# Optimization experiments

Hardware: AMD Instinct MI355X
Metric: run time of the kernel (lower is better)

## Reference

```python
import jax, jax.numpy as jnp
import numpy as np

H_SPLITS = [2, 3, 3]          # crpe_window {3:2, 5:3, 7:3}
K_SIZES = [3, 5, 7]
NUM_HEADS = 8
EPS = 1e-6


def dwconv(x, w, b, k):
    # x: (B,C,H,W), w: (C,1,k,k) depthwise, 'same' padding
    y = jax.lax.conv_general_dilated(
        x, w, (1, 1), [(k // 2, k // 2)] * 2,
        feature_group_count=x.shape[1],
        dimension_numbers=('NCHW', 'OIHW', 'NCHW'))
    return y + b[None, :, None, None]


def layernorm(x, g, b):
    m = jnp.mean(x, -1, keepdims=True)
    v = jnp.var(x, -1, keepdims=True)
    return (x - m) * jax.lax.rsqrt(v + EPS) * g + b


def conv_rel_pos_enc(q, v, ws, bs, H, W):
    # ConvRelPosEnc (MPViT style, no cls token): q * depthwise_conv(v)
    B, h, N, Ch = q.shape
    v_img = v.transpose(0, 1, 3, 2).reshape(B, h * Ch, H, W)  # B (h Ch) H W
    splits = np.cumsum([hs * Ch for hs in H_SPLITS])[:-1]
    parts = jnp.split(v_img, splits, axis=1)
    conv_v = jnp.concatenate(
        [dwconv(p, w, b, k) for p, w, b, k in zip(parts, ws, bs, K_SIZES)], axis=1)
    conv_v = conv_v.reshape(B, h, Ch, N).transpose(0, 1, 3, 2)
    return q * conv_v


def setup_inputs() -> dict:
    key = jax.random.key(0)
    B, H, W, C, nd, r, mr = 8, 64, 64, 320, 4, 2, 4
    h = NUM_HEADS
    N = H * W
    Ch = C // h
    hid = C // r
    ks = jax.random.split(key, 16)
    s = 0.02
    return {
        'x': jax.random.normal(ks[0], (B, N, C), jnp.float32),
        'domain_label': jax.nn.one_hot(jax.random.randint(ks[1], (B,), 0, nd), nd, dtype=jnp.float32),
        'cpe_w': jax.random.normal(ks[2], (C, 1, 3, 3), jnp.float32) * s,
        'cpe_b': jnp.zeros((C,), jnp.float32),
        'ln1_g': jnp.ones((C,), jnp.float32), 'ln1_b': jnp.zeros((C,), jnp.float32),
        'qkv_w': jax.random.normal(ks[3], (3 * C, C), jnp.float32) * s,
        'qkv_b': jnp.zeros((3 * C,), jnp.float32),
        'crpe_w3': jax.random.normal(ks[4], (2 * Ch, 1, 3, 3), jnp.float32) * s,
        'crpe_b3': jnp.zeros((2 * Ch,), jnp.float32),
        'crpe_w5': jax.random.normal(ks[5], (3 * Ch, 1, 5, 5), jnp.float32) * s,
        'crpe_b5': jnp.zeros((3 * Ch,), jnp.float32),
        'crpe_w7': jax.random.normal(ks[6], (3 * Ch, 1, 7, 7), jnp.float32) * s,
        'crpe_b7': jnp.zeros((3 * Ch,), jnp.float32),
        'dom_w1': jax.random.normal(ks[7], (hid, nd), jnp.float32) * s,
        'dom_b1': jnp.zeros((hid,), jnp.float32),
        'dom_w2': jax.random.normal(ks[8], (C, hid), jnp.float32) * s,
        'dom_b2': jnp.zeros((C,), jnp.float32),
        'proj_w': jax.random.normal(ks[9], (C, C), jnp.float32) * s,
        'proj_b': jnp.zeros((C,), jnp.float32),
        'ln2_g': jnp.ones((C,), jnp.float32), 'ln2_b': jnp.zeros((C,), jnp.float32),
        'mlp_w1': jax.random.normal(ks[10], (mr * C, C), jnp.float32) * s,
        'mlp_b1': jnp.zeros((mr * C,), jnp.float32),
        'mlp_w2': jax.random.normal(ks[11], (C, mr * C), jnp.float32) * s,
        'mlp_b2': jnp.zeros((C,), jnp.float32),
        'H': H, 'W': W,
    }


def reference(x, domain_label, cpe_w, cpe_b, ln1_g, ln1_b, qkv_w, qkv_b,
              crpe_w3, crpe_b3, crpe_w5, crpe_b5, crpe_w7, crpe_b7,
              dom_w1, dom_b1, dom_w2, dom_b2, proj_w, proj_b,
              ln2_g, ln2_b, mlp_w1, mlp_b1, mlp_w2, mlp_b2, H, W):
    B, N, C = x.shape
    h = NUM_HEADS
    Ch = C // h
    scale = Ch ** -0.5
    # ConvPosEnc: depthwise 3x3 conv + residual
    img = x.transpose(0, 2, 1).reshape(B, C, H, W)
    x = (dwconv(img, cpe_w, cpe_b, 3) + img).reshape(B, C, N).transpose(0, 2, 1)
    # FactorAtt_ConvRelPosEnc_Sup
    cur = layernorm(x, ln1_g, ln1_b)
    qkv = (cur @ qkv_w.T + qkv_b).reshape(B, N, 3, h, Ch).transpose(2, 0, 3, 1, 4)
    q, k, v = qkv[0], qkv[1], qkv[2]          # (B,h,N,Ch) each
    k_sm = jax.nn.softmax(k, axis=2)          # softmax over tokens
    kv = jnp.einsum('bhnk,bhnv->bhkv', k_sm, v)   # (B,h,Ch,Ch)
    fa = jnp.einsum('bhnk,bhkv->bhnv', q, kv)
    fa = scale * fa + conv_rel_pos_enc(
        q, v, (crpe_w3, crpe_w5, crpe_w7), (crpe_b3, crpe_b5, crpe_b7), H, W)
    # domain gate: MLP(one_hot) -> softmax over heads, broadcast over tokens
    d = jax.nn.relu(domain_label @ dom_w1.T + dom_b1) @ dom_w2.T + dom_b2  # (B,C)
    d = jax.nn.softmax(d.reshape(B, h, 1, Ch), axis=1)
    att = (d * fa).transpose(0, 2, 1, 3).reshape(B, N, C)
    x = x + (att @ proj_w.T + proj_b)
    # MLP (GELU, ratio 4)
    cur = layernorm(x, ln2_g, ln2_b)
    cur = jax.nn.gelu(cur @ mlp_w1.T + mlp_b1, approximate=False) @ mlp_w2.T + mlp_b2
    return x + cur
```

## Files before the change

kernel.cpp:

```cpp
#include <hip/hip_runtime.h>
#include <hip/hip_bf16.h>
#include <math.h>
#include <type_traits>

#define B_    8
#define Nn    4096
#define Cc    320
#define QS    1024
#define ATT_SCALE 0.15811388300841897f

typedef __attribute__((ext_vector_type(8))) short s8v;
typedef __attribute__((ext_vector_type(4))) float f4v;

__device__ __forceinline__ float bf2f(short u) {
    return __uint_as_float(((unsigned int)(unsigned short)u) << 16);
}
__device__ __forceinline__ short f2bf(float f) {
    return (short)__bfloat16_as_ushort(__float2bfloat16(f));
}

typedef const __attribute__((address_space(1))) unsigned int* gp1_t;
typedef __attribute__((address_space(3))) unsigned int* lp3_t;
__device__ __forceinline__ void gload16(const void* g, void* l) {
    __builtin_amdgcn_global_load_lds((gp1_t)g, (lp3_t)l, 16, 0, 0);
}

__global__ void cvt_pad(const float* __restrict__ s, __hip_bfloat16* __restrict__ d,
                        int rows_real, int K, int total) {
    int i = blockIdx.x * 256 + threadIdx.x;
    if (i >= total) return;
    int row = i / K;
    d[i] = (row < rows_real) ? __float2bfloat16(s[i]) : __float2bfloat16(0.f);
}

__global__ void ln_kernel(const float* __restrict__ x, const float* __restrict__ g,
                          const float* __restrict__ bt, __hip_bfloat16* __restrict__ out) {
    int bn = blockIdx.x;
    int lane = threadIdx.x;
    const float* row = x + (size_t)bn * Cc;
    float v[5];
    float s = 0.f, s2 = 0.f;
    #pragma unroll
    for (int i = 0; i < 5; ++i) {
        v[i] = row[lane + 64 * i];
        s += v[i];
        s2 += v[i] * v[i];
    }
    #pragma unroll
    for (int off = 32; off > 0; off >>= 1) {
        s  += __shfl_down(s, off);
        s2 += __shfl_down(s2, off);
    }
    s  = __shfl(s, 0);
    s2 = __shfl(s2, 0);
    float mean = s * (1.f / 320.f);
    float var  = s2 * (1.f / 320.f) - mean * mean;
    float rstd = rsqrtf(var + 1e-6f);
    __hip_bfloat16* orow = out + (size_t)bn * Cc;
    #pragma unroll
    for (int i = 0; i < 5; ++i) {
        int c = lane + 64 * i;
        orow[c] = __float2bfloat16((v[i] - mean) * rstd * g[c] + bt[c]);
    }
}

template<int ACT, int RES, int WF32, int WBF16>
__global__ __launch_bounds__(256) void gemm_mfma(
        const __hip_bfloat16* __restrict__ A, const __hip_bfloat16* __restrict__ W,
        const float* __restrict__ bias, const float* __restrict__ res,
        float* __restrict__ outf, __hip_bfloat16* __restrict__ outb,
        int K, int NS, int Nreal) {
    __shared__ __align__(16) short As[128 * 64];
    __shared__ __align__(16) short Bs[128 * 64];
    int tid = threadIdx.x;
    int m0 = blockIdx.x << 7;
    int n0 = blockIdx.y << 7;
    int w = tid >> 6, lane = tid & 63;
    int wr = w >> 1, wc = w & 1;
    int lrow = lane & 15, lk = lane >> 4;
    f4v acc[4][4];
    #pragma unroll
    for (int i = 0; i < 4; ++i)
        #pragma unroll
        for (int j = 0; j < 4; ++j) acc[i][j] = (f4v){0.f, 0.f, 0.f, 0.f};

    int srow = w * 32 + (lane >> 3);
    int slot = lane & 7;
    for (int k0 = 0; k0 < K; k0 += 64) {
        __syncthreads();
        #pragma unroll
        for (int i = 0; i < 4; ++i) {
            int row = srow + i * 8;
            int sk = (slot ^ (row & 7)) << 3;
            gload16(&A[(size_t)(m0 + row) * K + k0 + sk], &As[w * 2048 + i * 512]);
            gload16(&W[(size_t)(n0 + row) * K + k0 + sk], &Bs[w * 2048 + i * 512]);
        }
        __syncthreads();
        #pragma unroll
        for (int ks = 0; ks < 2; ++ks) {
            s8v af[4], bf[4];
            #pragma unroll
            for (int mi = 0; mi < 4; ++mi) {
                int row = wr * 64 + mi * 16 + lrow;
                int s = (ks * 4 + lk) ^ (row & 7);
                af[mi] = *reinterpret_cast<const s8v*>(&As[row * 64 + s * 8]);
            }
            #pragma unroll
            for (int ni = 0; ni < 4; ++ni) {
                int row = wc * 64 + ni * 16 + lrow;
                int s = (ks * 4 + lk) ^ (row & 7);
                bf[ni] = *reinterpret_cast<const s8v*>(&Bs[row * 64 + s * 8]);
            }
            #pragma unroll
            for (int mi = 0; mi < 4; ++mi)
                #pragma unroll
                for (int ni = 0; ni < 4; ++ni)
                    acc[mi][ni] = __builtin_amdgcn_mfma_f32_16x16x32_bf16(af[mi], bf[ni], acc[mi][ni], 0, 0, 0);
        }
    }
    #pragma unroll
    for (int mi = 0; mi < 4; ++mi) {
        #pragma unroll
        for (int ni = 0; ni < 4; ++ni) {
            int n = n0 + wc * 64 + ni * 16 + lrow;
            if (n >= Nreal) continue;
            float bv = bias[n];
            #pragma unroll
            for (int r = 0; r < 4; ++r) {
                int m = m0 + wr * 64 + mi * 16 + lk * 4 + r;
                float v = acc[mi][ni][r] + bv;
                if (RES) v += res[(size_t)m * NS + n];
                if (ACT == 1) v = 0.5f * v * (1.f + erff(v * 0.70710678118654752f));
                if (WF32) outf[(size_t)m * NS + n] = v;
                if (WBF16) outb[(size_t)m * NS + n] = __float2bfloat16(v);
            }
        }
    }
}

template<int KSZ, int EPI, typename ST>
__global__ __launch_bounds__(256) void dwconv_tile(
        const ST* __restrict__ src, int sstride, int scoff,
        const float* __restrict__ wts, const float* __restrict__ bias, int cbase, int ngrp,
        const float* __restrict__ aux0,
        const float* __restrict__ aux1,
        float* __restrict__ outf, __hip_bfloat16* __restrict__ outb) {
    constexpr int P = KSZ / 2;
    constexpr int S = 16 + 2 * P;
    __shared__ float vt[S * S * 8];
    __shared__ float ws_[8 * KSZ * KSZ];
    int blk = blockIdx.x;
    int tile = blk & 15;
    int g  = (blk >> 4) % ngrp;
    int b  = (blk >> 4) / ngrp;
    int ty0 = (tile >> 2) << 4;
    int tx0 = (tile & 3) << 4;
    int c0 = cbase + g * 8;
    int tid = threadIdx.x;
    for (int e = tid; e < 8 * KSZ * KSZ; e += 256)
        ws_[e] = wts[g * 8 * KSZ * KSZ + e];
    const ST* sb = src + (size_t)b * Nn * sstride + scoff + c0;
    for (int e = tid; e < S * S; e += 256) {
        int hy = e / S, hx = e % S;
        int gy = ty0 - P + hy, gx = tx0 - P + hx;
        float px8[8];
        #pragma unroll
        for (int j = 0; j < 8; ++j) px8[j] = 0.f;
        if ((unsigned)gy < 64u && (unsigned)gx < 64u) {
            const ST* p = &sb[(size_t)((gy << 6) + gx) * sstride];
            if constexpr (std::is_same<ST, float>::value) {
                float4 lo = reinterpret_cast<const float4*>(p)[0];
                float4 hi = reinterpret_cast<const float4*>(p)[1];
                px8[0] = lo.x; px8[1] = lo.y; px8[2] = lo.z; px8[3] = lo.w;
                px8[4] = hi.x; px8[5] = hi.y; px8[6] = hi.z; px8[7] = hi.w;
            } else {
                s8v v8 = *reinterpret_cast<const s8v*>(p);
                #pragma unroll
                for (int j = 0; j < 8; ++j) px8[j] = bf2f(v8[j]);
            }
        }
        #pragma unroll
        for (int j = 0; j < 8; ++j) vt[e * 8 + j] = px8[j];
    }
    __syncthreads();
    int cl  = tid & 7;
    int px  = (tid >> 3) & 15;
    int pyh = tid >> 7;
    int c = c0 + cl;
    float acc[8];
    float bval = bias[g * 8 + cl];
    #pragma unroll
    for (int j = 0; j < 8; ++j) acc[j] = bval;
    #pragma unroll
    for (int dx = 0; dx < KSZ; ++dx) {
        float col[8 + KSZ - 1];
        #pragma unroll
        for (int i = 0; i < 8 + KSZ - 1; ++i)
            col[i] = vt[((pyh * 8 + i) * S + (px + dx)) * 8 + cl];
        #pragma unroll
        for (int j = 0; j < 8; ++j)
            #pragma unroll
            for (int dy = 0; dy < KSZ; ++dy)
                acc[j] += col[j + dy] * ws_[cl * KSZ * KSZ + dy * KSZ + dx];
    }
    #pragma unroll
    for (int j = 0; j < 8; ++j) {
        int n = ((ty0 + pyh * 8 + j) << 6) + tx0 + px;
        size_t bn = (size_t)b * Nn + n;
        if (EPI == 0) {
            outf[bn * Cc + c] = acc[j] + aux0[bn * Cc + c];
        } else {
            float qv  = bf2f(((const short*)src)[bn * (size_t)sstride + c]);
            float fav = aux0[bn * Cc + c];
            float r = aux1[(size_t)b * Cc + c] * (ATT_SCALE * fav + qv * acc[j]);
            outb[bn * Cc + c] = __float2bfloat16(r);
        }
    }
}

__global__ __launch_bounds__(256) void kv_mfma(const __hip_bfloat16* __restrict__ qkv,
                                               float* __restrict__ kvp) {
    __shared__ short lds[4 * 2 * 48 * 66];
    int blk = blockIdx.x;
    int s = blk & 7;
    int bh = blk >> 3;
    int h = bh & 7, b = bh >> 3;
    int tid = threadIdx.x;
    int w = tid >> 6, lane = tid & 63;
    short* ke_t = lds + w * 2 * 48 * 66;
    short* vv_t = ke_t + 48 * 66;
    for (int e = lane; e < 8 * 66; e += 64) {
        ke_t[40 * 66 + e] = 0;
        vv_t[40 * 66 + e] = 0;
    }
    for (int n = lane; n < 66; n += 64) vv_t[40 * 66 + n] = (short)0x3F80;

    const short* kb = (const short*)qkv + (size_t)b * Nn * QS + 320 + h * 40;
    const short* vb = kb + 320;
    int col0 = lane & 15, kq = lane >> 4;
    f4v acc[3][3];
    #pragma unroll
    for (int i = 0; i < 3; ++i)
        #pragma unroll
        for (int j = 0; j < 3; ++j) acc[i][j] = (f4v){0.f, 0.f, 0.f, 0.f};

    for (int t = w; t < 8; t += 4) {
        int n0 = s * 512 + t * 64;
        for (int e = lane; e < 320; e += 64) {
            int nl = e / 5, oct = e % 5;
            size_t go = (size_t)(n0 + nl) * QS + oct * 8;
            s8v k8 = *reinterpret_cast<const s8v*>(kb + go);
            s8v v8 = *reinterpret_cast<const s8v*>(vb + go);
            #pragma unroll
            for (int j = 0; j < 8; ++j) {
                ke_t[(oct * 8 + j) * 66 + nl] = f2bf(__expf(bf2f(k8[j])));
                vv_t[(oct * 8 + j) * 66 + nl] = v8[j];
            }
        }
        __syncthreads();
        #pragma unroll
        for (int ks = 0; ks < 2; ++ks) {
            s8v af[3], bfr[3];
            #pragma unroll
            for (int mt = 0; mt < 3; ++mt)
                af[mt] = *reinterpret_cast<const s8v*>(ke_t + (mt * 16 + col0) * 66 + ks * 32 + kq * 8);
            #pragma unroll
            for (int nt = 0; nt < 3; ++nt)
                bfr[nt] = *reinterpret_cast<const s8v*>(vv_t + (nt * 16 + col0) * 66 + ks * 32 + kq * 8);
            #pragma unroll
            for (int mt = 0; mt < 3; ++mt)
                #pragma unroll
                for (int nt = 0; nt < 3; ++nt)
                    acc[mt][nt] = __builtin_amdgcn_mfma_f32_16x16x32_bf16(af[mt], bfr[nt], acc[mt][nt], 0, 0, 0);
        }
        __syncthreads();
    }
    float* red = (float*)lds;
    #pragma unroll
    for (int mt = 0; mt < 3; ++mt) {
        #pragma unroll
        for (int nt = 0; nt < 3; ++nt) {
            #pragma unroll
            for (int r = 0; r < 4; ++r) {
                int ch = mt * 16 + kq * 4 + r;
                int cv = nt * 16 + col0;
                if (ch < 40) red[w * 1920 + ch * 48 + cv] = acc[mt][nt][r];
            }
        }
    }
    __syncthreads();
    for (int p = tid; p < 1920; p += 256) {
        float sv = red[p] + red[1920 + p] + red[2 * 1920 + p] + red[3 * 1920 + p];
        kvp[(size_t)blk * 1920 + p] = sv;
    }
}

__global__ void kv_combine2(const float* __restrict__ kvp, float* __restrict__ kv) {
    int bh = blockIdx.x;
    int tid = threadIdx.x;
    __shared__ float sinv[40];
    if (tid < 40) {
        float S = 0.f;
        for (int s2 = 0; s2 < 8; ++s2)
            S += kvp[(size_t)(bh * 8 + s2) * 1920 + tid * 48 + 40];
        sinv[tid] = 1.f / S;
    }
    __syncthreads();
    for (int p = tid; p < 1600; p += 256) {
        int ch = p / 40, cv = p % 40;
        float v = 0.f;
        for (int s2 = 0; s2 < 8; ++s2)
            v += kvp[(size_t)(bh * 8 + s2) * 1920 + ch * 48 + cv];
        kv[(size_t)bh * 1600 + p] = v * sinv[ch];
    }
}

__global__ void dgate_kernel(const float* __restrict__ lbl, const float* __restrict__ w1,
                             const float* __restrict__ b1, const float* __restrict__ w2,
                             const float* __restrict__ b2, float* __restrict__ dg) {
    int b = blockIdx.x;
    int tid = threadIdx.x;
    __shared__ float hid[160];
    __shared__ float dd[320];
    if (tid < 160) {
        float a = b1[tid];
        for (int d = 0; d < 4; ++d) a += w1[tid * 4 + d] * lbl[b * 4 + d];
        hid[tid] = fmaxf(a, 0.f);
    }
    __syncthreads();
    float a = b2[tid];
    for (int j = 0; j < 160; ++j) a += w2[tid * 160 + j] * hid[j];
    dd[tid] = a;
    __syncthreads();
    if (tid < 40) {
        float M = -1e30f;
        for (int h2 = 0; h2 < 8; ++h2) M = fmaxf(M, dd[h2 * 40 + tid]);
        float S = 0.f;
        float e[8];
        for (int h2 = 0; h2 < 8; ++h2) { e[h2] = __expf(dd[h2 * 40 + tid] - M); S += e[h2]; }
        float inv = 1.f / S;
        for (int h2 = 0; h2 < 8; ++h2) dg[b * 320 + h2 * 40 + tid] = e[h2] * inv;
    }
}

__global__ __launch_bounds__(256) void fa_kernel(const __hip_bfloat16* __restrict__ qkv,
        const float* __restrict__ kvmat, float* __restrict__ fa) {
    __shared__ float kvs[1600];
    int blk = blockIdx.x;
    int chunk = blk & 15;
    int bh = blk >> 4;
    int h = bh & 7, b = bh >> 3;
    int tid = threadIdx.x;
    for (int e = tid; e < 1600; e += 256) kvs[e] = kvmat[(size_t)bh * 1600 + e];
    __syncthreads();
    int n = chunk * 256 + tid;
    const short* qr = (const short*)qkv + (size_t)(b * Nn + n) * QS + h * 40;
    float q[40];
    #pragma unroll
    for (int i = 0; i < 5; ++i) {
        s8v v8 = reinterpret_cast<const s8v*>(qr)[i];
        #pragma unroll
        for (int j = 0; j < 8; ++j) q[i * 8 + j] = bf2f(v8[j]);
    }
    float o[40];
    #pragma unroll
    for (int cv = 0; cv < 40; ++cv) o[cv] = 0.f;
    #pragma unroll
    for (int ch = 0; ch < 40; ++ch) {
        float qv = q[ch];
        #pragma unroll
        for (int cv = 0; cv < 40; ++cv)
            o[cv] += qv * kvs[ch * 40 + cv];
    }
    float* fr = fa + (size_t)(b * Nn + n) * 320 + h * 40;
    #pragma unroll
    for (int i = 0; i < 10; ++i)
        reinterpret_cast<float4*>(fr)[i] = make_float4(o[i * 4], o[i * 4 + 1], o[i * 4 + 2], o[i * 4 + 3]);
}

extern "C" void kernel_launch(void* const* d_in, const int* in_sizes, int n_in,
                              void* d_out, int out_size, void* d_ws, size_t ws_size,
                              hipStream_t stream) {
    const float* x     = (const float*)d_in[0];
    const float* lbl   = (const float*)d_in[1];
    const float* cpe_w = (const float*)d_in[2];
    const float* cpe_b = (const float*)d_in[3];
    const float* ln1g  = (const float*)d_in[4];
    const float* ln1b  = (const float*)d_in[5];
    const float* qkv_w = (const float*)d_in[6];
    const float* qkv_b = (const float*)d_in[7];
    const float* w3    = (const float*)d_in[8];
    const float* b3    = (const float*)d_in[9];
    const float* w5    = (const float*)d_in[10];
    const float* b5    = (const float*)d_in[11];
    const float* w7    = (const float*)d_in[12];
    const float* b7    = (const float*)d_in[13];
    const float* dw1   = (const float*)d_in[14];
    const float* db1   = (const float*)d_in[15];
    const float* dw2   = (const float*)d_in[16];
    const float* db2   = (const float*)d_in[17];
    const float* pw    = (const float*)d_in[18];
    const float* pb    = (const float*)d_in[19];
    const float* ln2g  = (const float*)d_in[20];
    const float* ln2b  = (const float*)d_in[21];
    const float* m1w   = (const float*)d_in[22];
    const float* m1b   = (const float*)d_in[23];
    const float* m2w   = (const float*)d_in[24];
    const float* m2b   = (const float*)d_in[25];
    float* out = (float*)d_out;

    float* ws = (float*)d_ws;
    float* x1   = ws; ws += 10485760;
    __hip_bfloat16* qkvb = (__hip_bfloat16*)ws; ws += 16777216;
    float* fa   = ws; ws += 20971520;
    __hip_bfloat16* gelub = (__hip_bfloat16*)fa;
    __hip_bfloat16* bb1   = (__hip_bfloat16*)ws; ws += 5242880;
    __hip_bfloat16* wb    = (__hip_bfloat16*)ws; ws += 675840;
    float* kvp  = ws; ws += 983040;
    float* kv   = ws; ws += 102400;
    float* dg   = ws; ws += 2560;
    __hip_bfloat16* wbq  = wb;
    __hip_bfloat16* wbp  = wbq  + 1024 * 320;
    __hip_bfloat16* wbm1 = wbp  + 384 * 320;
    __hip_bfloat16* wbm2 = wbm1 + 1280 * 320;

    cvt_pad<<<1280, 256, 0, stream>>>(qkv_w, wbq,  960, 320, 1024 * 320);
    cvt_pad<<<480,  256, 0, stream>>>(pw,    wbp,  320, 320, 384 * 320);
    cvt_pad<<<1600, 256, 0, stream>>>(m1w,   wbm1, 1280, 320, 1280 * 320);
    cvt_pad<<<1920, 256, 0, stream>>>(m2w,   wbm2, 320, 1280, 384 * 1280);
    dwconv_tile<3, 0, float><<<B_ * 40 * 16, 256, 0, stream>>>(
        x, 320, 0, cpe_w, cpe_b, 0, 40, x, nullptr, x1, nullptr);
    ln_kernel<<<B_ * Nn, 64, 0, stream>>>(x1, ln1g, ln1b, bb1);
    {
        dim3 g(256, 8);
        gemm_mfma<0, 0, 0, 1><<<g, 256, 0, stream>>>(bb1, wbq, qkv_b, nullptr, nullptr, qkvb,
                                                     320, QS, 960);
    }
    kv_mfma<<<512, 256, 0, stream>>>(qkvb, kvp);
    kv_combine2<<<64, 256, 0, stream>>>(kvp, kv);
    dgate_kernel<<<B_, 320, 0, stream>>>(lbl, dw1, db1, dw2, db2, dg);
    fa_kernel<<<B_ * 8 * 16, 256, 0, stream>>>(qkvb, kv, fa);
    dwconv_tile<3, 1, __hip_bfloat16><<<B_ * 10 * 16, 256, 0, stream>>>(
        qkvb, QS, 640, w3, b3, 0, 10, fa, dg, nullptr, bb1);
    dwconv_tile<5, 1, __hip_bfloat16><<<B_ * 15 * 16, 256, 0, stream>>>(
        qkvb, QS, 640, w5, b5, 80, 15, fa, dg, nullptr, bb1);
    dwconv_tile<7, 1, __hip_bfloat16><<<B_ * 15 * 16, 256, 0, stream>>>(
        qkvb, QS, 640, w7, b7, 200, 15, fa, dg, nullptr, bb1);
    {
        dim3 g(256, 3);
        gemm_mfma<0, 1, 1, 0><<<g, 256, 0, stream>>>(bb1, wbp, pb, x1, out, nullptr,
                                                     320, 320, 320);
    }
    ln_kernel<<<B_ * Nn, 64, 0, stream>>>(out, ln2g, ln2b, bb1);
    {
        dim3 g(256, 10);
        gemm_mfma<1, 0, 0, 1><<<g, 256, 0, stream>>>(bb1, wbm1, m1b, nullptr, nullptr, gelub,
                                                     320, 1280, 1280);
    }
    {
        dim3 g(256, 3);
        gemm_mfma<0, 1, 1, 0><<<g, 256, 0, stream>>>(gelub, wbm2, m2b, out, out, nullptr,
                                                     1280, 320, 320);
    }
}
```

Before: 360.3 us.

## Double-buffer GEMM LDS tiles, use tanh GELU, merge weight conversion kernels

The GEMM main loop now uses two LDS buffers, so the next K tile loads while the current one is computed, removing one barrier per iteration. The exact erf GELU in the epilogue becomes a tanh-based approximation built on __expf. The four weight fp32-to-bf16 conversion launches are merged into a single kernel. Double buffering doubles GEMM LDS use to 64 KB per block, which may lower occupancy. The tanh GELU changes numerics slightly compared with the reference's exact GELU.

```diff
diff --git a/kernel.cpp b/kernel.cpp
--- a/kernel.cpp
+++ b/kernel.cpp
@@ -18,6 +18,12 @@
 __device__ __forceinline__ short f2bf(float f) {
     return (short)__bfloat16_as_ushort(__float2bfloat16(f));
 }
+__device__ __forceinline__ float gelu_fast(float v) {
+    float u = v * (0.7978845608f + 0.0356774081f * v * v);
+    float e = __expf(2.f * u);
+    float t = 1.f - 2.f / (e + 1.f);
+    return 0.5f * v * (1.f + t);
+}
 
 typedef const __attribute__((address_space(1))) unsigned int* gp1_t;
 typedef __attribute__((address_space(3))) unsigned int* lp3_t;
@@ -25,12 +31,18 @@
     __builtin_amdgcn_global_load_lds((gp1_t)g, (lp3_t)l, 16, 0, 0);
 }
 
-__global__ void cvt_pad(const float* __restrict__ s, __hip_bfloat16* __restrict__ d,
-                        int rows_real, int K, int total) {
+__global__ void cvt_all(const float* __restrict__ s0, const float* __restrict__ s1,
+                        const float* __restrict__ s2, const float* __restrict__ s3,
+                        __hip_bfloat16* __restrict__ d) {
     int i = blockIdx.x * 256 + threadIdx.x;
-    if (i >= total) return;
-    int row = i / K;
-    d[i] = (row < rows_real) ? __float2bfloat16(s[i]) : __float2bfloat16(0.f);
+    if (i >= 1351680) return;
+    const float* s; int j, rows, K;
+    if (i < 327680)      { s = s0; j = i;          rows = 960;  K = 320; }
+    else if (i < 450560) { s = s1; j = i - 327680; rows = 320;  K = 320; }
+    else if (i < 860160) { s = s2; j = i - 450560; rows = 1280; K = 320; }
+    else                 { s = s3; j = i - 860160; rows = 320;  K = 1280; }
+    float v = (j / K < rows) ? s[j] : 0.f;
+    d[i] = __float2bfloat16(v);
 }
 
 __global__ void ln_kernel(const float* __restrict__ x, const float* __restrict__ g,
@@ -70,8 +82,8 @@
         const float* __restrict__ bias, const float* __restrict__ res,
         float* __restrict__ outf, __hip_bfloat16* __restrict__ outb,
         int K, int NS, int Nreal) {
-    __shared__ __align__(16) short As[128 * 64];
-    __shared__ __align__(16) short Bs[128 * 64];
+    __shared__ __align__(16) short As[2][128 * 64];
+    __shared__ __align__(16) short Bs[2][128 * 64];
     int tid = threadIdx.x;
     int m0 = blockIdx.x << 7;
     int n0 = blockIdx.y << 7;
@@ -86,16 +98,17 @@
 
     int srow = w * 32 + (lane >> 3);
     int slot = lane & 7;
-    for (int k0 = 0; k0 < K; k0 += 64) {
-        __syncthreads();
+
+    auto STAGE = [&](int buf, int k0) {
         #pragma unroll
         for (int i = 0; i < 4; ++i) {
             int row = srow + i * 8;
             int sk = (slot ^ (row & 7)) << 3;
-            gload16(&A[(size_t)(m0 + row) * K + k0 + sk], &As[w * 2048 + i * 512]);
-            gload16(&W[(size_t)(n0 + row) * K + k0 + sk], &Bs[w * 2048 + i * 512]);
-        }
-        __syncthreads();
+            gload16(&A[(size_t)(m0 + row) * K + k0 + sk], &As[buf][w * 2048 + i * 512]);
+            gload16(&W[(size_t)(n0 + row) * K + k0 + sk], &Bs[buf][w * 2048 + i * 512]);
+        }
+    };
+    auto COMPUTE = [&](int buf) {
         #pragma unroll
         for (int ks = 0; ks < 2; ++ks) {
             s8v af[4], bf[4];
@@ -103,13 +116,13 @@
             for (int mi = 0; mi < 4; ++mi) {
                 int row = wr * 64 + mi * 16 + lrow;
                 int s = (ks * 4 + lk) ^ (row & 7);
-                af[mi] = *reinterpret_cast<const s8v*>(&As[row * 64 + s * 8]);
+                af[mi] = *reinterpret_cast<const s8v*>(&As[buf][row * 64 + s * 8]);
             }
             #pragma unroll
             for (int ni = 0; ni < 4; ++ni) {
                 int row = wc * 64 + ni * 16 + lrow;
                 int s = (ks * 4 + lk) ^ (row & 7);
-                bf[ni] = *reinterpret_cast<const s8v*>(&Bs[row * 64 + s * 8]);
+                bf[ni] = *reinterpret_cast<const s8v*>(&Bs[buf][row * 64 + s * 8]);
             }
             #pragma unroll
             for (int mi = 0; mi < 4; ++mi)
@@ -117,7 +130,18 @@
                 for (int ni = 0; ni < 4; ++ni)
                     acc[mi][ni] = __builtin_amdgcn_mfma_f32_16x16x32_bf16(af[mi], bf[ni], acc[mi][ni], 0, 0, 0);
         }
-    }
+    };
+
+    STAGE(0, 0);
+    __syncthreads();
+    int cur = 0;
+    for (int k0 = 0; k0 < K; k0 += 64) {
+        if (k0 + 64 < K) STAGE(cur ^ 1, k0 + 64);
+        COMPUTE(cur);
+        __syncthreads();
+        cur ^= 1;
+    }
+
     #pragma unroll
     for (int mi = 0; mi < 4; ++mi) {
         #pragma unroll
@@ -130,7 +154,7 @@
                 int m = m0 + wr * 64 + mi * 16 + lk * 4 + r;
                 float v = acc[mi][ni][r] + bv;
                 if (RES) v += res[(size_t)m * NS + n];
-                if (ACT == 1) v = 0.5f * v * (1.f + erff(v * 0.70710678118654752f));
+                if (ACT == 1) v = gelu_fast(v);
                 if (WF32) outf[(size_t)m * NS + n] = v;
                 if (WBF16) outb[(size_t)m * NS + n] = __float2bfloat16(v);
             }
@@ -424,10 +448,7 @@
     __hip_bfloat16* wbm1 = wbp  + 384 * 320;
     __hip_bfloat16* wbm2 = wbm1 + 1280 * 320;
 
-    cvt_pad<<<1280, 256, 0, stream>>>(qkv_w, wbq,  960, 320, 1024 * 320);
-    cvt_pad<<<480,  256, 0, stream>>>(pw,    wbp,  320, 320, 384 * 320);
-    cvt_pad<<<1600, 256, 0, stream>>>(m1w,   wbm1, 1280, 320, 1280 * 320);
-    cvt_pad<<<1920, 256, 0, stream>>>(m2w,   wbm2, 320, 1280, 384 * 1280);
+    cvt_all<<<5280, 256, 0, stream>>>(qkv_w, pw, m1w, m2w, wb);
     dwconv_tile<3, 0, float><<<B_ * 40 * 16, 256, 0, stream>>>(
         x, 320, 0, cpe_w, cpe_b, 0, 40, x, nullptr, x1, nullptr);
     ln_kernel<<<B_ * Nn, 64, 0, stream>>>(x1, ln1g, ln1b, bb1);
```

Result: slower. 399.6 us (+10.9%).
